# Optimization experiments

Measured on AMD Instinct MI355X. Metric: run time of the kernel, lower is better.

The kernel has to match this reference:

```python
import jax, jax.numpy as jnp
import numpy as np

NQ = 4          # n_qubits == hidden_dim (required for gate broadcasting)
D = 256         # embed_dim
H = 4           # num_heads
HD = D // H     # head_dim
V = 32000       # vocab
TAG = 64        # tagset_size
B, T = 16, 512


def _apply_rx(state, theta, wire):
    # state: (B, 2,2,2,2) complex64; theta: (B,) angles. RX = [[c,-is],[-is,c]], c=cos(t/2)
    half = theta * 0.5
    c = jnp.cos(half).reshape(-1, 1, 1, 1).astype(state.real.dtype)
    s = jnp.sin(half).reshape(-1, 1, 1, 1).astype(state.real.dtype)
    st = jnp.moveaxis(state, wire + 1, 1)
    a, b = st[:, 0], st[:, 1]
    st2 = jnp.stack([c * a - 1j * s * b, c * b - 1j * s * a], axis=1)
    return jnp.moveaxis(st2, 1, wire + 1)


def _apply_cnot(state, ctrl, tgt):
    st = jnp.moveaxis(state, (ctrl + 1, tgt + 1), (1, 2))
    st2 = jnp.stack([st[:, 0], st[:, 1, ::-1]], axis=1)  # flip target when ctrl=1
    return jnp.moveaxis(st2, (1, 2), (ctrl + 1, tgt + 1))


def _qlayer(angles, thetas):
    # angles: (B, NQ) data-encoding RX angles; thetas: (NQ,) trainable RX angles
    bsz = angles.shape[0]
    state = jnp.zeros((bsz,) + (2,) * NQ, jnp.complex64)
    state = state.at[(slice(None),) + (0,) * NQ].set(1.0)
    for w in range(NQ):
        state = _apply_rx(state, angles[:, w], w)
    for w in range(NQ):
        state = _apply_rx(state, jnp.broadcast_to(thetas[w], (bsz,)), w)
    for w in range(NQ - 1):
        state = _apply_cnot(state, w, w + 1)
    state = _apply_cnot(state, NQ - 1, 0)
    probs = state.real ** 2 + state.imag ** 2
    pm = jnp.array([1.0, -1.0], probs.dtype)
    outs = [
        jnp.sum(probs * pm.reshape((1,) + tuple(2 if i == w else 1 for i in range(NQ))),
                axis=tuple(range(1, NQ + 1)))
        for w in range(NQ)
    ]
    return jnp.stack(outs, axis=-1)  # (B, NQ) PauliZ expectations


def _forward(sentence, emb, Wq, bq, Wk, bk, Wv, bv, Wo, bo,
             Wf, bf, thf, Wi, bi, thi, Wg, bg, thg, Wo2, bo2, tho, Wt, bt):
    x = emb[sentence]  # (B, T, D)
    Bc, Tc, _ = x.shape
    # multi-head self-attention
    q = (x @ Wq.T + bq).reshape(Bc, Tc, H, HD).transpose(0, 2, 1, 3)
    k = (x @ Wk.T + bk).reshape(Bc, Tc, H, HD).transpose(0, 2, 1, 3)
    v = (x @ Wv.T + bv).reshape(Bc, Tc, H, HD).transpose(0, 2, 1, 3)
    scores = jnp.einsum('bhqd,bhkd->bhqk', q, k) / (HD ** 0.5)
    attn = jax.nn.softmax(scores, axis=-1)
    o = jnp.einsum('bhqk,bhkd->bhqd', attn, v).transpose(0, 2, 1, 3).reshape(Bc, Tc, D)
    attn_out = o @ Wo.T + bo  # (B, T, D)

    # quantum LSTM over time via scan
    def step(carry, x_t):
        hx, cx = carry  # (B, NQ) each
        comb = jnp.concatenate([x_t, hx], axis=-1)  # (B, D+NQ)
        f = jax.nn.sigmoid(_qlayer(comb @ Wf.T + bf, thf))
        i = jax.nn.sigmoid(_qlayer(comb @ Wi.T + bi, thi))
        g = jnp.tanh(_qlayer(comb @ Wg.T + bg, thg))
        oo = jax.nn.sigmoid(_qlayer(comb @ Wo2.T + bo2, tho))
        cx = f * cx + i * g
        hx = oo * jnp.tanh(cx)
        return (hx, cx), hx

    h0 = jnp.zeros((Bc, NQ), x.dtype)
    _, hs = jax.lax.scan(step, (h0, h0), attn_out.transpose(1, 0, 2))  # (T, B, NQ)
    lstm_out = hs.transpose(1, 0, 2)  # (B, T, NQ)
    logits = lstm_out @ Wt.T + bt
    return jax.nn.log_softmax(logits, axis=-1)


def setup_inputs() -> dict:
    key = jax.random.key(0)
    ks = jax.random.split(key, 24)
    n = lambda k, shp, sc=0.02: (jax.random.normal(k, shp, jnp.float32) * sc)
    DQ = D + NQ
    return {
        'sentence': jax.random.randint(ks[0], (B, T), 0, V),
        'emb': n(ks[1], (V, D), 1.0),
        'Wq': n(ks[2], (D, D)), 'bq': jnp.zeros((D,), jnp.float32),
        'Wk': n(ks[3], (D, D)), 'bk': jnp.zeros((D,), jnp.float32),
        'Wv': n(ks[4], (D, D)), 'bv': jnp.zeros((D,), jnp.float32),
        'Wo': n(ks[5], (D, D)), 'bo': jnp.zeros((D,), jnp.float32),
        'Wf': n(ks[6], (NQ, DQ), 0.05), 'bf': jnp.zeros((NQ,), jnp.float32),
        'thf': jax.random.uniform(ks[7], (NQ,), jnp.float32, 0.0, 2 * np.pi),
        'Wi': n(ks[8], (NQ, DQ), 0.05), 'bi': jnp.zeros((NQ,), jnp.float32),
        'thi': jax.random.uniform(ks[9], (NQ,), jnp.float32, 0.0, 2 * np.pi),
        'Wg': n(ks[10], (NQ, DQ), 0.05), 'bg': jnp.zeros((NQ,), jnp.float32),
        'thg': jax.random.uniform(ks[11], (NQ,), jnp.float32, 0.0, 2 * np.pi),
        'Wo2': n(ks[12], (NQ, DQ), 0.05), 'bo2': jnp.zeros((NQ,), jnp.float32),
        'tho': jax.random.uniform(ks[13], (NQ,), jnp.float32, 0.0, 2 * np.pi),
        'Wt': n(ks[14], (TAG, NQ), 0.1), 'bt': jnp.zeros((TAG,), jnp.float32),
    }


def reference(sentence, emb, Wq, bq, Wk, bk, Wv, bv, Wo, bo,
              Wf, bf, thf, Wi, bi, thi, Wg, bg, thg, Wo2, bo2, tho, Wt, bt):
    return _forward(sentence, emb, Wq, bq, Wk, bk, Wv, bv, Wo, bo,
                    Wf, bf, thf, Wi, bi, thi, Wg, bg, thg, Wo2, bo2, tho, Wt, bt)
```

## Files before the change

kernel.cpp:

```cpp
#include <hip/hip_runtime.h>
#include <hip/hip_bf16.h>

#define NB 16
#define NT 512
#define ND 256
#define NH 4
#define NHD 64
#define NTAG 64

typedef short bf16x8 __attribute__((ext_vector_type(8)));
typedef float f32x4 __attribute__((ext_vector_type(4)));
union LdsVec { uint4 u; bf16x8 v; };

#define INV2PI 0.15915494309189535f

__device__ __forceinline__ float ldf(const void* p, int isbf, long i) {
  return isbf ? __bfloat162float(((const __hip_bfloat16*)p)[i])
              : ((const float*)p)[i];
}
__device__ __forceinline__ unsigned short bfbits(float f) {
  __hip_bfloat16 h = __float2bfloat16(f);
  union { __hip_bfloat16 h; unsigned short s; } u{h};
  return u.s;
}
__device__ __forceinline__ unsigned int pack2(float a, float b) {
  return ((unsigned int)bfbits(b) << 16) | bfbits(a);
}

template <int CTRL>
__device__ __forceinline__ float dppf(float v) {
  return __int_as_float(
      __builtin_amdgcn_update_dpp(0, __float_as_int(v), CTRL, 0xF, 0xF, false));
}

__device__ __forceinline__ float frcp(float x) {
#if __has_builtin(__builtin_amdgcn_rcpf)
  return __builtin_amdgcn_rcpf(x);
#else
  float r; asm("v_rcp_f32 %0, %1" : "=v"(r) : "v"(x)); return r;
#endif
}
__device__ __forceinline__ float fexp2(float x) {
#if __has_builtin(__builtin_amdgcn_exp2f)
  return __builtin_amdgcn_exp2f(x);
#else
  float r; asm("v_exp_f32 %0, %1" : "=v"(r) : "v"(x)); return r;
#endif
}
__device__ __forceinline__ float fcosr(float x) {
#if __has_builtin(__builtin_amdgcn_cosf)
  return __builtin_amdgcn_cosf(x);
#else
  float r; asm("v_cos_f32 %0, %1" : "=v"(r) : "v"(x)); return r;
#endif
}

__device__ __forceinline__ int detect_isbf(const void* buf, int nview) {
  __shared__ int s_big;
  if (threadIdx.x == 0) s_big = 0;
  __syncthreads();
  const __hip_bfloat16* p = (const __hip_bfloat16*)buf;
  int big = 0;
  for (int i = threadIdx.x; i < nview; i += blockDim.x) {
    float v = __bfloat162float(p[i]);
    if (fabsf(v) > 1e4f) big = 1;
  }
  if (big) atomicOr(&s_big, 1);
  __syncthreads();
  return s_big ? 0 : 1;
}

#define AST 264
#define BST 40
__global__ __launch_bounds__(256) void k_qkvc(
    const int* __restrict__ sent, const void* emb,
    const void* Wq, const void* Wk, const void* Wv,
    const void* bq, const void* bk, const void* bv,
    const void* Wo, const void* bo,
    const void* Wf, const void* Wi, const void* Wg, const void* Wo2,
    const void* bF, const void* bI, const void* bG, const void* bO,
    const void* thF, const void* thI, const void* thG, const void* thO,
    __hip_bfloat16* Qbf, __hip_bfloat16* Kbf, __hip_bfloat16* Vtbf,
    __hip_bfloat16* __restrict__ Mbf, float* __restrict__ P) {
  __shared__ __align__(16) unsigned short SH[64 * AST + 4 * 64 * BST];
  unsigned short* AS = SH;
  unsigned short* BS = SH + 64 * AST;
  int z = blockIdx.z;
  int tid = threadIdx.x;

  if (z == 3) {
    if (blockIdx.x >= 4) return;
    float (*WGs)[256] = (float(*)[256])SH;
    float* cs = (float*)BS;
    int isbf = detect_isbf(Wo, 4096);
    for (int e = tid; e < 4096; e += 256) {
      int oi = e >> 8, j = e & 255;
      int gate = oi >> 2, w = oi & 3;
      const void* Ws = (gate == 0) ? Wf : (gate == 1) ? Wi : (gate == 2) ? Wg : Wo2;
      WGs[oi][j] = ldf(Ws, isbf, (long)w * 260 + j);
    }
    __syncthreads();
    if (tid < 64) {
      int d = blockIdx.x * 64 + tid;
      float m[16];
#pragma unroll
      for (int oi = 0; oi < 16; ++oi) m[oi] = 0.f;
#pragma unroll 4
      for (int j = 0; j < 256; ++j) {
        float wo = ldf(Wo, isbf, (long)j * 256 + d);
#pragma unroll
        for (int oi = 0; oi < 16; ++oi) m[oi] += WGs[oi][j] * wo;
      }
#pragma unroll
      for (int oi = 0; oi < 16; ++oi)
        Mbf[oi * 256 + d] = __float2bfloat16(m[oi]);
    }
    if (tid < 16) {
      int gate = tid >> 2, w = tid & 3;
      float cc = 0.f;
      for (int j = 0; j < 256; ++j) cc += WGs[tid][j] * ldf(bo, isbf, j);
      const void* bsel = (gate == 0) ? bF : (gate == 1) ? bI : (gate == 2) ? bG : bO;
      const void* tsel = (gate == 0) ? thF : (gate == 1) ? thI : (gate == 2) ? thG : thO;
      cs[tid] = (cc + ldf(bsel, isbf, w) + ldf(tsel, isbf, w)) * INV2PI;
    }
    __syncthreads();
    long pb = (long)blockIdx.x * 32768;
    for (int i = tid; i < 32768; i += 256) P[pb + i] = cs[i & 15];
    return;
  }

  const void* W = (z == 0) ? Wq : (z == 1) ? Wk : Wv;
  const void* Bb = (z == 0) ? bq : (z == 1) ? bk : bv;
  __hip_bfloat16* O = (z == 0) ? Qbf : (z == 1) ? Kbf : Vtbf;
  int isbf = detect_isbf(W, 1024);

  int rowbase = blockIdx.x * 64;
  int wave = tid >> 6, lane = tid & 63;
  int li = lane & 15, quad = lane >> 4;
  int colbase = wave * 64;
  unsigned short* Bw = &BS[wave * 64 * BST];

  const float* Wf32 = (const float*)W;
  const __hip_bfloat16* Wb16 = (const __hip_bfloat16*)W;
  long wrow = (long)(colbase + lane) * 256;

  float4 bf[8];
  uint4 bb4[4];
  if (isbf) {
#pragma unroll
    for (int j = 0; j < 4; ++j) bb4[j] = *(const uint4*)&Wb16[wrow + j * 8];
  } else {
#pragma unroll
    for (int j = 0; j < 8; ++j) bf[j] = *(const float4*)&Wf32[wrow + j * 4];
  }

  {
    int srow = tid >> 2;
    int sc = (tid & 3) * 64;
    long tok = (long)sent[rowbase + srow];
    if (isbf) {
      const __hip_bfloat16* eb = (const __hip_bfloat16*)emb + tok * 256 + sc;
#pragma unroll
      for (int j = 0; j < 8; ++j)
        *(uint4*)&AS[srow * AST + sc + j * 8] = *(const uint4*)&eb[j * 8];
    } else {
      const float* ef = (const float*)emb + tok * 256 + sc;
#pragma unroll
      for (int j = 0; j < 8; ++j) {
        float4 lo = *(const float4*)&ef[j * 8];
        float4 hi = *(const float4*)&ef[j * 8 + 4];
        uint4 pk;
        pk.x = pack2(lo.x, lo.y); pk.y = pack2(lo.z, lo.w);
        pk.z = pack2(hi.x, hi.y); pk.w = pack2(hi.z, hi.w);
        *(uint4*)&AS[srow * AST + sc + j * 8] = pk;
      }
    }
  }
  __syncthreads();

  f32x4 acc[4][4];
#pragma unroll
  for (int mt = 0; mt < 4; ++mt)
#pragma unroll
    for (int nt = 0; nt < 4; ++nt) acc[mt][nt] = (f32x4){0.f, 0.f, 0.f, 0.f};

#pragma unroll
  for (int k0 = 0; k0 < 256; k0 += 32) {
    if (isbf) {
#pragma unroll
      for (int j = 0; j < 4; ++j)
        *(uint4*)&Bw[lane * BST + j * 8] = bb4[j];
    } else {
#pragma unroll
      for (int j = 0; j < 4; ++j) {
        uint4 pk;
        pk.x = pack2(bf[2 * j].x, bf[2 * j].y);
        pk.y = pack2(bf[2 * j].z, bf[2 * j].w);
        pk.z = pack2(bf[2 * j + 1].x, bf[2 * j + 1].y);
        pk.w = pack2(bf[2 * j + 1].z, bf[2 * j + 1].w);
        *(uint4*)&Bw[lane * BST + j * 8] = pk;
      }
    }
    if (k0 < 224) {
      if (isbf) {
#pragma unroll
        for (int j = 0; j < 4; ++j)
          bb4[j] = *(const uint4*)&Wb16[wrow + k0 + 32 + j * 8];
      } else {
#pragma unroll
        for (int j = 0; j < 8; ++j)
          bf[j] = *(const float4*)&Wf32[wrow + k0 + 32 + j * 4];
      }
    }
    LdsVec a[4], b[4];
#pragma unroll
    for (int mt = 0; mt < 4; ++mt)
      a[mt].u = *(const uint4*)&AS[(mt * 16 + li) * AST + k0 + quad * 8];
#pragma unroll
    for (int nt = 0; nt < 4; ++nt)
      b[nt].u = *(const uint4*)&Bw[(nt * 16 + li) * BST + quad * 8];
#pragma unroll
    for (int mt = 0; mt < 4; ++mt)
#pragma unroll
      for (int nt = 0; nt < 4; ++nt)
        acc[mt][nt] = __builtin_amdgcn_mfma_f32_16x16x32_bf16(
            a[mt].v, b[nt].v, acc[mt][nt], 0, 0, 0);
  }

  __syncthreads();
  if (z == 2) {
#pragma unroll
    for (int nt = 0; nt < 4; ++nt) {
      int col = colbase + nt * 16 + li;
      float bias = ldf(Bb, isbf, col);
#pragma unroll
      for (int mt = 0; mt < 4; ++mt)
#pragma unroll
        for (int reg = 0; reg < 4; ++reg)
          SH[col * 72 + mt * 16 + quad * 4 + reg] =
              bfbits(acc[mt][nt][reg] + bias);
    }
  } else {
#pragma unroll
    for (int nt = 0; nt < 4; ++nt) {
      int col = colbase + nt * 16 + li;
      float bias = ldf(Bb, isbf, col);
#pragma unroll
      for (int mt = 0; mt < 4; ++mt)
#pragma unroll
        for (int reg = 0; reg < 4; ++reg)
          SH[(mt * 16 + quad * 4 + reg) * AST + col] =
              bfbits(acc[mt][nt][reg] + bias);
    }
  }
  __syncthreads();
  int bb2 = blockIdx.x >> 3, ttb = (blockIdx.x & 7) * 64;
  if (z == 2) {
#pragma unroll
    for (int j = 0; j < 8; ++j) {
      int e = tid + j * 256;
      int hdcol = e >> 3, c8 = (e & 7) * 8;
      uint4 v = *(const uint4*)&SH[hdcol * 72 + c8];
      *(uint4*)((__hip_bfloat16*)O +
                ((long)(bb2 * 4 + (hdcol >> 6)) * 64 + (hdcol & 63)) * 512 +
                ttb + c8) = v;
    }
  } else {
#pragma unroll
    for (int j = 0; j < 8; ++j) {
      int e = tid + j * 256;
      int row = e >> 5, c8e = (e & 31) * 8;
      int h = c8e >> 6, hd = c8e & 63;
      uint4 v = *(const uint4*)&SH[row * AST + c8e];
      *(uint4*)((__hip_bfloat16*)O +
                ((long)(bb2 * 4 + h) * 512 + ttb + row) * 64 + hd) = v;
    }
  }
}

#define LSTR 72
__global__ __launch_bounds__(256) void k_attn(const __hip_bfloat16* __restrict__ Qg,
                                              const __hip_bfloat16* __restrict__ Kg,
                                              const __hip_bfloat16* __restrict__ Vtg,
                                              const __hip_bfloat16* __restrict__ Mbf,
                                              float* __restrict__ P) {
  __shared__ __align__(16) unsigned short Qs[64 * LSTR];
  __shared__ __align__(16) unsigned short Ks[64 * LSTR];
  __shared__ __align__(16) unsigned short Vts[64 * LSTR];
  __shared__ __align__(16) unsigned short Ps[64 * LSTR];
  int tid = threadIdx.x;
  int bh = blockIdx.x, qt = blockIdx.y;
  int wave = tid >> 6, lane = tid & 63, li = lane & 15, quad = lane >> 4;

  const __hip_bfloat16* Qb = Qg + ((long)bh * 512 + qt * 64) * 64;
#pragma unroll
  for (int c = 0; c < 2; ++c) {
    int idx = tid + c * 256;
    int r = idx >> 3, c8 = (idx & 7) * 8;
    *(uint4*)&Qs[r * LSTR + c8] = *(const uint4*)&Qb[(long)r * 64 + c8];
  }

  f32x4 accO[4];
  float mrow[4], lrow[4];
#pragma unroll
  for (int i = 0; i < 4; ++i) {
    accO[i] = (f32x4){0.f, 0.f, 0.f, 0.f};
    mrow[i] = -1e30f; lrow[i] = 0.f;
  }

  for (int kt = 0; kt < 8; ++kt) {
    __syncthreads();
    const __hip_bfloat16* Kb = Kg + ((long)bh * 512 + kt * 64) * 64;
#pragma unroll
    for (int c = 0; c < 2; ++c) {
      int idx = tid + c * 256;
      int r = idx >> 3, c8 = (idx & 7) * 8;
      *(uint4*)&Ks[r * LSTR + c8] = *(const uint4*)&Kb[(long)r * 64 + c8];
      *(uint4*)&Vts[r * LSTR + c8] =
          *(const uint4*)&Vtg[((long)bh * 64 + r) * 512 + kt * 64 + c8];
    }
    __syncthreads();

    f32x4 s[4];
#pragma unroll
    for (int nb = 0; nb < 4; ++nb) s[nb] = (f32x4){0.f, 0.f, 0.f, 0.f};
#pragma unroll
    for (int nb = 0; nb < 4; ++nb)
#pragma unroll
      for (int kc = 0; kc < 2; ++kc) {
        LdsVec a, b;
        a.u = *(const uint4*)&Qs[(wave * 16 + li) * LSTR + kc * 32 + quad * 8];
        b.u = *(const uint4*)&Ks[(nb * 16 + li) * LSTR + kc * 32 + quad * 8];
        s[nb] = __builtin_amdgcn_mfma_f32_16x16x32_bf16(a.v, b.v, s[nb], 0, 0, 0);
      }
#pragma unroll
    for (int nb = 0; nb < 4; ++nb) s[nb] *= 0.125f;

#pragma unroll
    for (int reg = 0; reg < 4; ++reg) {
      float rm = fmaxf(fmaxf(s[0][reg], s[1][reg]), fmaxf(s[2][reg], s[3][reg]));
      rm = fmaxf(rm, __shfl_xor(rm, 1));
      rm = fmaxf(rm, __shfl_xor(rm, 2));
      rm = fmaxf(rm, __shfl_xor(rm, 4));
      rm = fmaxf(rm, __shfl_xor(rm, 8));
      float mnew = fmaxf(mrow[reg], rm);
      float alpha = __expf(mrow[reg] - mnew);
      mrow[reg] = mnew;
      float psum = 0.f;
#pragma unroll
      for (int nb = 0; nb < 4; ++nb) {
        float p = __expf(s[nb][reg] - mnew);
        psum += p;
        Ps[(wave * 16 + quad * 4 + reg) * LSTR + nb * 16 + li] = bfbits(p);
      }
      psum += __shfl_xor(psum, 1);
      psum += __shfl_xor(psum, 2);
      psum += __shfl_xor(psum, 4);
      psum += __shfl_xor(psum, 8);
      lrow[reg] = lrow[reg] * alpha + psum;
#pragma unroll
      for (int db = 0; db < 4; ++db) accO[db][reg] *= alpha;
    }
    __syncthreads();

#pragma unroll
    for (int db = 0; db < 4; ++db)
#pragma unroll
      for (int kc = 0; kc < 2; ++kc) {
        LdsVec a, b;
        a.u = *(const uint4*)&Ps[(wave * 16 + li) * LSTR + kc * 32 + quad * 8];
        b.u = *(const uint4*)&Vts[(db * 16 + li) * LSTR + kc * 32 + quad * 8];
        accO[db] = __builtin_amdgcn_mfma_f32_16x16x32_bf16(a.v, b.v, accO[db], 0, 0, 0);
      }
  }

  int batch = bh >> 2, head = bh & 3;
  __syncthreads();
  if (tid < 128) {
    int r = tid >> 3, c8 = (tid & 7) * 8;
    *(uint4*)&Qs[r * LSTR + c8] = *(const uint4*)&Mbf[r * 256 + head * 64 + c8];
  }
#pragma unroll
  for (int reg = 0; reg < 4; ++reg) {
    float inv = 1.f / lrow[reg];
#pragma unroll
    for (int db = 0; db < 4; ++db)
      Ps[(wave * 16 + quad * 4 + reg) * LSTR + db * 16 + li] =
          bfbits(accO[db][reg] * inv);
  }
  __syncthreads();
  f32x4 pacc = (f32x4){0.f, 0.f, 0.f, 0.f};
#pragma unroll
  for (int kc = 0; kc < 2; ++kc) {
    LdsVec a, b;
    a.u = *(const uint4*)&Ps[(wave * 16 + li) * LSTR + kc * 32 + quad * 8];
    b.u = *(const uint4*)&Qs[li * LSTR + kc * 32 + quad * 8];
    pacc = __builtin_amdgcn_mfma_f32_16x16x32_bf16(a.v, b.v, pacc, 0, 0, 0);
  }
  long pbase = (long)(batch >> 2) * 32768 + (batch & 3) * 16 + li;
#pragma unroll
  for (int reg = 0; reg < 4; ++reg) {
    int t = qt * 64 + wave * 16 + quad * 4 + reg;
    atomicAdd(&P[pbase + (long)t * 64], pacc[reg] * INV2PI);
  }
}

#define SWEEPS 4
#define CHUNK 16
#define NCH 32

template <bool DIRB>
__device__ __forceinline__ void scan_sweeps(
    const float* __restrict__ Pb,
    int c, int G, int w,
    float rr0, float rr1, float rr2, float rr3,
    float kk, float e1, float mkm1,
    int s0, int s1, int s2, int s3,
    float (*bH)[NCH + 1][4], float (*bC)[NCH + 1][4],
    float* __restrict__ hsb) {
  float pcv[CHUNK];
#pragma unroll
  for (int j = 0; j < CHUNK; ++j)
    pcv[j] = Pb[(long)(c * CHUNK + j) * 64];

#pragma unroll 1
  for (int s = 0; s < SWEEPS; ++s) {
    int rd = s & 1, wr = rd ^ 1;
    float h0 = bH[rd][c][0], h1 = bH[rd][c][1];
    float h2 = bH[rd][c][2], h3 = bH[rd][c][3];
    float cx = bC[rd][c][w];
    float hx = 0.f;
#pragma unroll
    for (int u = 0; u < CHUNK; ++u) {
      float pc = pcv[u];
      float d01 = __builtin_fmaf(rr1, h1, __builtin_fmaf(rr0, h0, pc));
      float d23 = __builtin_fmaf(rr3, h3, rr2 * h2);
      float a = d01 + d23;
      float cth = fcosr(a);
      float c0 = dppf<0x00>(cth), c1 = dppf<0x55>(cth);
      float c2 = dppf<0xAA>(cth), c3 = dppf<0xFF>(cth);
      float p01 = c0 * c1, z23 = c2 * c3;
      float v = (w == 0) ? c1 * z23 : (w == 1) ? p01
              : (w == 2) ? p01 * c2 : p01 * z23;
      float val = __builtin_fmaf(kk, frcp(1.f + fexp2(e1 * v)), mkm1);
      float ra = dppf<0x124>(val);
      float rb = dppf<0x128>(val);
      float rc = dppf<0x12C>(val);
      float rot1 = DIRB ? ra : rc;
      float rot3 = DIRB ? rc : ra;
      float f = (s0 == 0) ? val : (s0 == 1) ? rot1 : (s0 == 2) ? rb : rot3;
      float i = (s1 == 0) ? val : (s1 == 1) ? rot1 : (s1 == 2) ? rb : rot3;
      float g = (s2 == 0) ? val : (s2 == 1) ? rot1 : (s2 == 2) ? rb : rot3;
      float o = (s3 == 0) ? val : (s3 == 1) ? rot1 : (s3 == 2) ? rb : rot3;
      cx = __builtin_fmaf(f, cx, i * g);
      float rt = frcp(1.f + fexp2(-2.88539008f * cx));
      hx = __builtin_fmaf(o + o, rt, -o);
      h0 = dppf<0x00>(hx); h1 = dppf<0x55>(hx);
      h2 = dppf<0xAA>(hx); h3 = dppf<0xFF>(hx);
      if (G == 0) hsb[(c * CHUNK + u) * 4 + w] = hx;
    }
    if (G == 0) {
      bH[wr][c + 1][w] = hx;
      bC[wr][c + 1][w] = cx;
    }
    __syncthreads();
  }
}

__global__ __launch_bounds__(512) void k_scanf(const float* __restrict__ P,
                                               const void* Wf, const void* Wi,
                                               const void* Wg, const void* Wo2,
                                               const void* Wt, const void* Bt,
                                               void* outp) {
  __shared__ float bH[2][NCH + 1][4];
  __shared__ float bC[2][NCH + 1][4];
  __shared__ __align__(16) float hsb[512 * 4];
  __shared__ float sWt[256];
  __shared__ float sBt[64];
  int tid = threadIdx.x;
  int b = blockIdx.x;
  int c = tid >> 4;
  int l16 = tid & 15;
  int G = l16 >> 2, w = l16 & 3;
  int lane = tid & 63;

  if (tid < 2 * (NCH + 1) * 4) {
    ((float*)bH)[tid] = 0.f;
    ((float*)bC)[tid] = 0.f;
  }

  const __hip_bfloat16* pw = (const __hip_bfloat16*)Wf;
  int big = 0;
  for (int i = lane; i < 1040; i += 64) {
    float v = __bfloat162float(pw[i]);
    if (fabsf(v) > 1e4f) big = 1;
  }
  int isbf = (__ballot(big) == 0ULL) ? 1 : 0;

  if (tid < 256) sWt[tid] = ldf(Wt, isbf, tid);
  else if (tid < 320) sBt[tid - 256] = ldf(Bt, isbf, tid - 256);

  int got = __builtin_amdgcn_update_dpp(0, lane, 0x124, 0xF, 0xF, false);
  int dir = __shfl((got == 9) ? 1 : 0, 5);
  const void* Wsel = (G == 0) ? Wf : (G == 1) ? Wi : (G == 2) ? Wg : Wo2;
  float rr0 = ldf(Wsel, isbf, (long)w * 260 + 256 + 0) * INV2PI;
  float rr1 = ldf(Wsel, isbf, (long)w * 260 + 256 + 1) * INV2PI;
  float rr2 = ldf(Wsel, isbf, (long)w * 260 + 256 + 2) * INV2PI;
  float rr3 = ldf(Wsel, isbf, (long)w * 260 + 256 + 3) * INV2PI;
  float kk = (G == 2) ? 2.f : 1.f;
  float e1 = -kk * 1.44269504f;
  float mkm1 = 1.f - kk;
  int s0 = (0 - G) & 3, s1 = (1 - G) & 3, s2 = (2 - G) & 3, s3 = (3 - G) & 3;

  const float* Pb = P + (long)(b >> 2) * 32768 + (b & 3) * 16 + l16;
  __syncthreads();

  if (dir)
    scan_sweeps<true>(Pb, c, G, w, rr0, rr1, rr2, rr3,
                      kk, e1, mkm1, s0, s1, s2, s3, bH, bC, hsb);
  else
    scan_sweeps<false>(Pb, c, G, w, rr0, rr1, rr2, rr3,
                       kk, e1, mkm1, s0, s1, s2, s3, bH, bC, hsb);

  float h0 = hsb[tid * 4 + 0], h1 = hsb[tid * 4 + 1];
  float h2 = hsb[tid * 4 + 2], h3 = hsb[tid * 4 + 3];
  float lg[64];
  float mx = -1e30f;
#pragma unroll
  for (int j = 0; j < 64; ++j) {
    float v = sBt[j]
            + h0 * sWt[j * 4 + 0] + h1 * sWt[j * 4 + 1]
            + h2 * sWt[j * 4 + 2] + h3 * sWt[j * 4 + 3];
    lg[j] = v;
    mx = fmaxf(mx, v);
  }
  float ssum = 0.f;
#pragma unroll
  for (int j = 0; j < 64; ++j) ssum += __expf(lg[j] - mx);
  float sub = mx + __logf(ssum);
  long rbase = ((long)b * 512 + tid) * 64;
  if (isbf) {
    __hip_bfloat16* ob = (__hip_bfloat16*)outp;
#pragma unroll
    for (int j0 = 0; j0 < 8; ++j0) {
      uint4 pk;
      pk.x = pack2(lg[j0 * 8 + 0] - sub, lg[j0 * 8 + 1] - sub);
      pk.y = pack2(lg[j0 * 8 + 2] - sub, lg[j0 * 8 + 3] - sub);
      pk.z = pack2(lg[j0 * 8 + 4] - sub, lg[j0 * 8 + 5] - sub);
      pk.w = pack2(lg[j0 * 8 + 6] - sub, lg[j0 * 8 + 7] - sub);
      *(uint4*)(ob + rbase + j0 * 8) = pk;
    }
  } else {
    float* of = (float*)outp;
#pragma unroll
    for (int j0 = 0; j0 < 16; ++j0) {
      float4 v4;
      v4.x = lg[j0 * 4 + 0] - sub; v4.y = lg[j0 * 4 + 1] - sub;
      v4.z = lg[j0 * 4 + 2] - sub; v4.w = lg[j0 * 4 + 3] - sub;
      *(float4*)(of + rbase + j0 * 4) = v4;
    }
  }
}

extern "C" void kernel_launch(void* const* d_in, const int* in_sizes, int n_in,
                              void* d_out, int out_size, void* d_ws, size_t ws_size,
                              hipStream_t stream) {
  const int* sent = (const int*)d_in[0];
  const void* emb = d_in[1];
  const void* Wq = d_in[2];  const void* bq = d_in[3];
  const void* Wk = d_in[4];  const void* bk = d_in[5];
  const void* Wv = d_in[6];  const void* bv = d_in[7];
  const void* Wo = d_in[8];  const void* bo = d_in[9];
  const void* Wf = d_in[10]; const void* bF = d_in[11]; const void* thF = d_in[12];
  const void* Wi = d_in[13]; const void* bI = d_in[14]; const void* thI = d_in[15];
  const void* Wg = d_in[16]; const void* bG = d_in[17]; const void* thG = d_in[18];
  const void* Wo2 = d_in[19]; const void* bO = d_in[20]; const void* thO = d_in[21];
  const void* Wt = d_in[22]; const void* Bt = d_in[23];

  float* base = (float*)((char*)d_ws + 256);
  __hip_bfloat16* Mbf = (__hip_bfloat16*)base;
  __hip_bfloat16* Qbf  = (__hip_bfloat16*)(base + 4096);
  __hip_bfloat16* Kbf  = (__hip_bfloat16*)(base + 4096 + 1048576);
  __hip_bfloat16* Vtbf = (__hip_bfloat16*)(base + 4096 + 2097152);
  float* Pp = base + 4096 + 3145728;

  dim3 gq(128, 1, 4);
  k_qkvc<<<gq, 256, 0, stream>>>(sent, emb, Wq, Wk, Wv, bq, bk, bv, Wo, bo,
                                 Wf, Wi, Wg, Wo2, bF, bI, bG, bO,
                                 thF, thI, thG, thO, Qbf, Kbf, Vtbf, Mbf, Pp);
  dim3 ga(64, 8, 1);
  k_attn<<<ga, 256, 0, stream>>>(Qbf, Kbf, Vtbf, Mbf, Pp);
  k_scanf<<<16, 512, 0, stream>>>(Pp, Wf, Wi, Wg, Wo2, Wt, Bt, d_out);
}
```

Baseline: 231.9 us.

## Fuse K/V projection into attention kernel with per-head LDS-resident K and V

The K and V projections move out of the QKV kernel into a new attention kernel, with one 512-thread block per (batch, head). Each block computes the full K and transposed V for its head into XOR-swizzled LDS, then runs flash attention over all 512 queries from that resident K/V. This drops the global write and re-read of K and V and one launch's worth of work. The cost is only 64 blocks with about 144KB of LDS each, so GPU occupancy is much lower and the whole attention runs on a quarter of the CUs.

```diff
diff --git a/kernel.cpp b/kernel.cpp
--- a/kernel.cpp
+++ b/kernel.cpp
@@ -13,6 +13,7 @@
 union LdsVec { uint4 u; bf16x8 v; };
 
 #define INV2PI 0.15915494309189535f
+#define FSW(r, bc) ((bc) ^ (((r) & 7) << 4))
 
 __device__ __forceinline__ float ldf(const void* p, int isbf, long i) {
   return isbf ? __bfloat162float(((const __hip_bfloat16*)p)[i])
@@ -72,23 +73,21 @@
 
 #define AST 264
 #define BST 40
-__global__ __launch_bounds__(256) void k_qkvc(
+__global__ __launch_bounds__(256) void k_qc(
     const int* __restrict__ sent, const void* emb,
-    const void* Wq, const void* Wk, const void* Wv,
-    const void* bq, const void* bk, const void* bv,
+    const void* Wq, const void* bq,
     const void* Wo, const void* bo,
     const void* Wf, const void* Wi, const void* Wg, const void* Wo2,
     const void* bF, const void* bI, const void* bG, const void* bO,
     const void* thF, const void* thI, const void* thG, const void* thO,
-    __hip_bfloat16* Qbf, __hip_bfloat16* Kbf, __hip_bfloat16* Vtbf,
+    __hip_bfloat16* __restrict__ Qbf,
     __hip_bfloat16* __restrict__ Mbf, float* __restrict__ P) {
   __shared__ __align__(16) unsigned short SH[64 * AST + 4 * 64 * BST];
   unsigned short* AS = SH;
   unsigned short* BS = SH + 64 * AST;
-  int z = blockIdx.z;
   int tid = threadIdx.x;
 
-  if (z == 3) {
+  if (blockIdx.z == 1) {
     if (blockIdx.x >= 4) return;
     float (*WGs)[256] = (float(*)[256])SH;
     float* cs = (float*)BS;
@@ -129,19 +128,15 @@
     return;
   }
 
-  const void* W = (z == 0) ? Wq : (z == 1) ? Wk : Wv;
-  const void* Bb = (z == 0) ? bq : (z == 1) ? bk : bv;
-  __hip_bfloat16* O = (z == 0) ? Qbf : (z == 1) ? Kbf : Vtbf;
-  int isbf = detect_isbf(W, 1024);
-
+  int isbf = detect_isbf(Wq, 1024);
   int rowbase = blockIdx.x * 64;
   int wave = tid >> 6, lane = tid & 63;
   int li = lane & 15, quad = lane >> 4;
   int colbase = wave * 64;
   unsigned short* Bw = &BS[wave * 64 * BST];
 
-  const float* Wf32 = (const float*)W;
-  const __hip_bfloat16* Wb16 = (const __hip_bfloat16*)W;
+  const float* Wf32 = (const float*)Wq;
+  const __hip_bfloat16* Wb16 = (const __hip_bfloat16*)Wq;
   long wrow = (long)(colbase + lane) * 256;
 
   float4 bf[8];
@@ -228,180 +223,258 @@
   }
 
   __syncthreads();
-  if (z == 2) {
-#pragma unroll
-    for (int nt = 0; nt < 4; ++nt) {
-      int col = colbase + nt * 16 + li;
-      float bias = ldf(Bb, isbf, col);
-#pragma unroll
-      for (int mt = 0; mt < 4; ++mt)
-#pragma unroll
-        for (int reg = 0; reg < 4; ++reg)
-          SH[col * 72 + mt * 16 + quad * 4 + reg] =
-              bfbits(acc[mt][nt][reg] + bias);
-    }
-  } else {
-#pragma unroll
-    for (int nt = 0; nt < 4; ++nt) {
-      int col = colbase + nt * 16 + li;
-      float bias = ldf(Bb, isbf, col);
-#pragma unroll
-      for (int mt = 0; mt < 4; ++mt)
-#pragma unroll
-        for (int reg = 0; reg < 4; ++reg)
-          SH[(mt * 16 + quad * 4 + reg) * AST + col] =
-              bfbits(acc[mt][nt][reg] + bias);
-    }
+#pragma unroll
+  for (int nt = 0; nt < 4; ++nt) {
+    int col = colbase + nt * 16 + li;
+    float bias = ldf(bq, isbf, col);
+#pragma unroll
+    for (int mt = 0; mt < 4; ++mt)
+#pragma unroll
+      for (int reg = 0; reg < 4; ++reg)
+        SH[(mt * 16 + quad * 4 + reg) * AST + col] =
+            bfbits(acc[mt][nt][reg] + bias);
   }
   __syncthreads();
   int bb2 = blockIdx.x >> 3, ttb = (blockIdx.x & 7) * 64;
-  if (z == 2) {
-#pragma unroll
-    for (int j = 0; j < 8; ++j) {
-      int e = tid + j * 256;
-      int hdcol = e >> 3, c8 = (e & 7) * 8;
-      uint4 v = *(const uint4*)&SH[hdcol * 72 + c8];
-      *(uint4*)((__hip_bfloat16*)O +
-                ((long)(bb2 * 4 + (hdcol >> 6)) * 64 + (hdcol & 63)) * 512 +
-                ttb + c8) = v;
-    }
-  } else {
-#pragma unroll
-    for (int j = 0; j < 8; ++j) {
-      int e = tid + j * 256;
-      int row = e >> 5, c8e = (e & 31) * 8;
-      int h = c8e >> 6, hd = c8e & 63;
-      uint4 v = *(const uint4*)&SH[row * AST + c8e];
-      *(uint4*)((__hip_bfloat16*)O +
-                ((long)(bb2 * 4 + h) * 512 + ttb + row) * 64 + hd) = v;
-    }
-  }
-}
-
-#define LSTR 72
-__global__ __launch_bounds__(256) void k_attn(const __hip_bfloat16* __restrict__ Qg,
-                                              const __hip_bfloat16* __restrict__ Kg,
-                                              const __hip_bfloat16* __restrict__ Vtg,
-                                              const __hip_bfloat16* __restrict__ Mbf,
-                                              float* __restrict__ P) {
-  __shared__ __align__(16) unsigned short Qs[64 * LSTR];
-  __shared__ __align__(16) unsigned short Ks[64 * LSTR];
-  __shared__ __align__(16) unsigned short Vts[64 * LSTR];
-  __shared__ __align__(16) unsigned short Ps[64 * LSTR];
+#pragma unroll
+  for (int j = 0; j < 8; ++j) {
+    int e = tid + j * 256;
+    int row = e >> 5, c8e = (e & 31) * 8;
+    int h = c8e >> 6, hd = c8e & 63;
+    uint4 v = *(const uint4*)&SH[row * AST + c8e];
+    *(uint4*)(Qbf + ((long)(bb2 * 4 + h) * 512 + ttb + row) * 64 + hd) = v;
+  }
+}
+
+__global__ __launch_bounds__(512) void k_fat(
+    const int* __restrict__ sent, const void* emb,
+    const void* Wk, const void* Wv, const void* bk, const void* bv,
+    const __hip_bfloat16* __restrict__ Qg,
+    const __hip_bfloat16* __restrict__ Mbf, float* __restrict__ P) {
+  __shared__ __align__(16) unsigned char Ks[512 * 128];
+  __shared__ __align__(16) unsigned char Vts[64 * 1024];
+  __shared__ __align__(16) unsigned char AW[32 * 512];
   int tid = threadIdx.x;
-  int bh = blockIdx.x, qt = blockIdx.y;
   int wave = tid >> 6, lane = tid & 63, li = lane & 15, quad = lane >> 4;
-
-  const __hip_bfloat16* Qb = Qg + ((long)bh * 512 + qt * 64) * 64;
-#pragma unroll
-  for (int c = 0; c < 2; ++c) {
-    int idx = tid + c * 256;
-    int r = idx >> 3, c8 = (idx & 7) * 8;
-    *(uint4*)&Qs[r * LSTR + c8] = *(const uint4*)&Qb[(long)r * 64 + c8];
-  }
-
-  f32x4 accO[4];
-  float mrow[4], lrow[4];
-#pragma unroll
-  for (int i = 0; i < 4; ++i) {
-    accO[i] = (f32x4){0.f, 0.f, 0.f, 0.f};
-    mrow[i] = -1e30f; lrow[i] = 0.f;
-  }
-
-  for (int kt = 0; kt < 8; ++kt) {
+  int bh = blockIdx.x, batch = bh >> 2, head = bh & 3;
+  int isbf = detect_isbf(Wk, 1024);
+
+  int srow = tid >> 4, sseg = tid & 15;
+
+  int kvw = (wave < 4) ? wave : wave - 4;
+  int dloc = kvw * 16 + li;
+  int col = head * 64 + dloc;
+  const void* Wsel = (wave < 4) ? Wk : Wv;
+  float bias = ldf((wave < 4) ? bk : bv, isbf, col);
+  uint4 wf[8];
+  {
+    long wr = (long)col * 256;
+    if (isbf) {
+      const __hip_bfloat16* wp = (const __hip_bfloat16*)Wsel;
+#pragma unroll
+      for (int k0 = 0; k0 < 8; ++k0)
+        wf[k0] = *(const uint4*)&wp[wr + k0 * 32 + quad * 8];
+    } else {
+      const float* wp = (const float*)Wsel;
+#pragma unroll
+      for (int k0 = 0; k0 < 8; ++k0) {
+        const float* pp = wp + wr + k0 * 32 + quad * 8;
+        float4 lo = *(const float4*)pp, hi = *(const float4*)(pp + 4);
+        wf[k0].x = pack2(lo.x, lo.y); wf[k0].y = pack2(lo.z, lo.w);
+        wf[k0].z = pack2(hi.x, hi.y); wf[k0].w = pack2(hi.z, hi.w);
+      }
+    }
+  }
+
+  uint4 sa0, sa1;
+  {
+    long tok = (long)sent[batch * 512 + srow];
+    if (isbf) {
+      const __hip_bfloat16* ep = (const __hip_bfloat16*)emb + tok * 256;
+      sa0 = *(const uint4*)&ep[sseg * 8];
+      sa1 = *(const uint4*)&ep[(sseg + 16) * 8];
+    } else {
+      const float* ep = (const float*)emb + tok * 256;
+      const float* p0 = ep + sseg * 8;
+      float4 lo = *(const float4*)p0, hi = *(const float4*)(p0 + 4);
+      sa0.x = pack2(lo.x, lo.y); sa0.y = pack2(lo.z, lo.w);
+      sa0.z = pack2(hi.x, hi.y); sa0.w = pack2(hi.z, hi.w);
+      const float* p1 = ep + (sseg + 16) * 8;
+      lo = *(const float4*)p1; hi = *(const float4*)(p1 + 4);
+      sa1.x = pack2(lo.x, lo.y); sa1.y = pack2(lo.z, lo.w);
+      sa1.z = pack2(hi.x, hi.y); sa1.w = pack2(hi.z, hi.w);
+    }
+  }
+#pragma unroll 1
+  for (int hc = 0; hc < 16; ++hc) {
     __syncthreads();
-    const __hip_bfloat16* Kb = Kg + ((long)bh * 512 + kt * 64) * 64;
-#pragma unroll
-    for (int c = 0; c < 2; ++c) {
-      int idx = tid + c * 256;
-      int r = idx >> 3, c8 = (idx & 7) * 8;
-      *(uint4*)&Ks[r * LSTR + c8] = *(const uint4*)&Kb[(long)r * 64 + c8];
-      *(uint4*)&Vts[r * LSTR + c8] =
-          *(const uint4*)&Vtg[((long)bh * 64 + r) * 512 + kt * 64 + c8];
+    *(uint4*)(AW + srow * 512 + FSW(srow, sseg * 16)) = sa0;
+    *(uint4*)(AW + srow * 512 + FSW(srow, (sseg + 16) * 16)) = sa1;
+    if (hc < 15) {
+      long tok = (long)sent[batch * 512 + (hc + 1) * 32 + srow];
+      if (isbf) {
+        const __hip_bfloat16* ep = (const __hip_bfloat16*)emb + tok * 256;
+        sa0 = *(const uint4*)&ep[sseg * 8];
+        sa1 = *(const uint4*)&ep[(sseg + 16) * 8];
+      } else {
+        const float* ep = (const float*)emb + tok * 256;
+        const float* p0 = ep + sseg * 8;
+        float4 lo = *(const float4*)p0, hi = *(const float4*)(p0 + 4);
+        sa0.x = pack2(lo.x, lo.y); sa0.y = pack2(lo.z, lo.w);
+        sa0.z = pack2(hi.x, hi.y); sa0.w = pack2(hi.z, hi.w);
+        const float* p1 = ep + (sseg + 16) * 8;
+        lo = *(const float4*)p1; hi = *(const float4*)(p1 + 4);
+        sa1.x = pack2(lo.x, lo.y); sa1.y = pack2(lo.z, lo.w);
+        sa1.z = pack2(hi.x, hi.y); sa1.w = pack2(hi.z, hi.w);
+      }
     }
     __syncthreads();
-
-    f32x4 s[4];
-#pragma unroll
-    for (int nb = 0; nb < 4; ++nb) s[nb] = (f32x4){0.f, 0.f, 0.f, 0.f};
-#pragma unroll
-    for (int nb = 0; nb < 4; ++nb)
-#pragma unroll
-      for (int kc = 0; kc < 2; ++kc) {
-        LdsVec a, b;
-        a.u = *(const uint4*)&Qs[(wave * 16 + li) * LSTR + kc * 32 + quad * 8];
-        b.u = *(const uint4*)&Ks[(nb * 16 + li) * LSTR + kc * 32 + quad * 8];
-        s[nb] = __builtin_amdgcn_mfma_f32_16x16x32_bf16(a.v, b.v, s[nb], 0, 0, 0);
-      }
-#pragma unroll
-    for (int nb = 0; nb < 4; ++nb) s[nb] *= 0.125f;
-
-#pragma unroll
-    for (int reg = 0; reg < 4; ++reg) {
-      float rm = fmaxf(fmaxf(s[0][reg], s[1][reg]), fmaxf(s[2][reg], s[3][reg]));
-      rm = fmaxf(rm, __shfl_xor(rm, 1));
-      rm = fmaxf(rm, __shfl_xor(rm, 2));
-      rm = fmaxf(rm, __shfl_xor(rm, 4));
-      rm = fmaxf(rm, __shfl_xor(rm, 8));
-      float mnew = fmaxf(mrow[reg], rm);
-      float alpha = __expf(mrow[reg] - mnew);
-      mrow[reg] = mnew;
-      float psum = 0.f;
-#pragma unroll
-      for (int nb = 0; nb < 4; ++nb) {
-        float p = __expf(s[nb][reg] - mnew);
-        psum += p;
-        Ps[(wave * 16 + quad * 4 + reg) * LSTR + nb * 16 + li] = bfbits(p);
-      }
-      psum += __shfl_xor(psum, 1);
-      psum += __shfl_xor(psum, 2);
-      psum += __shfl_xor(psum, 4);
-      psum += __shfl_xor(psum, 8);
-      lrow[reg] = lrow[reg] * alpha + psum;
-#pragma unroll
-      for (int db = 0; db < 4; ++db) accO[db][reg] *= alpha;
-    }
-    __syncthreads();
-
-#pragma unroll
-    for (int db = 0; db < 4; ++db)
-#pragma unroll
-      for (int kc = 0; kc < 2; ++kc) {
-        LdsVec a, b;
-        a.u = *(const uint4*)&Ps[(wave * 16 + li) * LSTR + kc * 32 + quad * 8];
-        b.u = *(const uint4*)&Vts[(db * 16 + li) * LSTR + kc * 32 + quad * 8];
-        accO[db] = __builtin_amdgcn_mfma_f32_16x16x32_bf16(a.v, b.v, accO[db], 0, 0, 0);
-      }
-  }
-
-  int batch = bh >> 2, head = bh & 3;
+    int r0 = hc * 32;
+    f32x4 acc0 = (f32x4){0.f, 0.f, 0.f, 0.f};
+    f32x4 acc1 = (f32x4){0.f, 0.f, 0.f, 0.f};
+#pragma unroll
+    for (int k0 = 0; k0 < 8; ++k0) {
+      LdsVec a0, a1, b;
+      a0.u = *(const uint4*)(AW + li * 512 + FSW(li, k0 * 64 + quad * 16));
+      a1.u = *(const uint4*)(AW + (16 + li) * 512 + FSW(16 + li, k0 * 64 + quad * 16));
+      b.u = wf[k0];
+      acc0 = __builtin_amdgcn_mfma_f32_16x16x32_bf16(a0.v, b.v, acc0, 0, 0, 0);
+      acc1 = __builtin_amdgcn_mfma_f32_16x16x32_bf16(a1.v, b.v, acc1, 0, 0, 0);
+    }
+    if (wave < 4) {
+#pragma unroll
+      for (int reg = 0; reg < 4; ++reg) {
+        int t0 = r0 + quad * 4 + reg, t1 = t0 + 16;
+        *(unsigned short*)(Ks + t0 * 128 + FSW(t0, 2 * dloc)) =
+            bfbits(acc0[reg] + bias);
+        *(unsigned short*)(Ks + t1 * 128 + FSW(t1, 2 * dloc)) =
+            bfbits(acc1[reg] + bias);
+      }
+    } else {
+      uint2 p0, p1;
+      p0.x = pack2(acc0[0] + bias, acc0[1] + bias);
+      p0.y = pack2(acc0[2] + bias, acc0[3] + bias);
+      p1.x = pack2(acc1[0] + bias, acc1[1] + bias);
+      p1.y = pack2(acc1[2] + bias, acc1[3] + bias);
+      int t0 = r0 + quad * 4, t1 = t0 + 16;
+      *(uint2*)(Vts + dloc * 1024 + FSW(dloc, 2 * t0)) = p0;
+      *(uint2*)(Vts + dloc * 1024 + FSW(dloc, 2 * t1)) = p1;
+    }
+  }
   __syncthreads();
-  if (tid < 128) {
-    int r = tid >> 3, c8 = (tid & 7) * 8;
-    *(uint4*)&Qs[r * LSTR + c8] = *(const uint4*)&Mbf[r * 256 + head * 64 + c8];
-  }
-#pragma unroll
-  for (int reg = 0; reg < 4; ++reg) {
-    float inv = 1.f / lrow[reg];
-#pragma unroll
-    for (int db = 0; db < 4; ++db)
-      Ps[(wave * 16 + quad * 4 + reg) * LSTR + db * 16 + li] =
-          bfbits(accO[db][reg] * inv);
-  }
-  __syncthreads();
-  f32x4 pacc = (f32x4){0.f, 0.f, 0.f, 0.f};
-#pragma unroll
-  for (int kc = 0; kc < 2; ++kc) {
-    LdsVec a, b;
-    a.u = *(const uint4*)&Ps[(wave * 16 + li) * LSTR + kc * 32 + quad * 8];
-    b.u = *(const uint4*)&Qs[li * LSTR + kc * 32 + quad * 8];
-    pacc = __builtin_amdgcn_mfma_f32_16x16x32_bf16(a.v, b.v, pacc, 0, 0, 0);
-  }
+
+  unsigned char* rg = AW + wave * 2048;
+  uint4 mf0 = *(const uint4*)&Mbf[li * 256 + head * 64 + 0 * 32 + quad * 8];
+  uint4 mf1 = *(const uint4*)&Mbf[li * 256 + head * 64 + 1 * 32 + quad * 8];
   long pbase = (long)(batch >> 2) * 32768 + (batch & 3) * 16 + li;
-#pragma unroll
-  for (int reg = 0; reg < 4; ++reg) {
-    int t = qt * 64 + wave * 16 + quad * 4 + reg;
-    atomicAdd(&P[pbase + (long)t * 64], pacc[reg] * INV2PI);
+
+#pragma unroll 1
+  for (int qh = 0; qh < 2; ++qh) {
+    uint4 qf[2][2];
+#pragma unroll
+    for (int mt = 0; mt < 2; ++mt)
+#pragma unroll
+      for (int kc = 0; kc < 2; ++kc)
+        qf[mt][kc] = *(const uint4*)&Qg[((long)bh * 512 + wave * 64 + qh * 32 +
+                                         mt * 16 + li) * 64 + kc * 32 + quad * 8];
+    f32x4 accO[2][4];
+    float mrow[2][4], lrow[2][4];
+#pragma unroll
+    for (int mt = 0; mt < 2; ++mt)
+#pragma unroll
+      for (int db = 0; db < 4; ++db) {
+        accO[mt][db] = (f32x4){0.f, 0.f, 0.f, 0.f};
+        mrow[mt][db] = -1e30f; lrow[mt][db] = 0.f;
+      }
+
+#pragma unroll 1
+    for (int kt = 0; kt < 8; ++kt) {
+      f32x4 s[2][4];
+#pragma unroll
+      for (int mt = 0; mt < 2; ++mt)
+#pragma unroll
+        for (int nb = 0; nb < 4; ++nb) s[mt][nb] = (f32x4){0.f, 0.f, 0.f, 0.f};
+#pragma unroll
+      for (int nb = 0; nb < 4; ++nb)
+#pragma unroll
+        for (int kc = 0; kc < 2; ++kc) {
+          int tr = kt * 64 + nb * 16 + li;
+          LdsVec b, a0, a1;
+          b.u = *(const uint4*)(Ks + tr * 128 + FSW(tr, kc * 64 + quad * 16));
+          a0.u = qf[0][kc]; a1.u = qf[1][kc];
+          s[0][nb] = __builtin_amdgcn_mfma_f32_16x16x32_bf16(a0.v, b.v, s[0][nb], 0, 0, 0);
+          s[1][nb] = __builtin_amdgcn_mfma_f32_16x16x32_bf16(a1.v, b.v, s[1][nb], 0, 0, 0);
+        }
+#pragma unroll
+      for (int mt = 0; mt < 2; ++mt) {
+#pragma unroll
+        for (int nb = 0; nb < 4; ++nb) s[mt][nb] *= 0.125f;
+#pragma unroll
+        for (int reg = 0; reg < 4; ++reg) {
+          float rm = fmaxf(fmaxf(s[mt][0][reg], s[mt][1][reg]),
+                           fmaxf(s[mt][2][reg], s[mt][3][reg]));
+          rm = fmaxf(rm, __shfl_xor(rm, 1));
+          rm = fmaxf(rm, __shfl_xor(rm, 2));
+          rm = fmaxf(rm, __shfl_xor(rm, 4));
+          rm = fmaxf(rm, __shfl_xor(rm, 8));
+          float mnew = fmaxf(mrow[mt][reg], rm);
+          float alpha = __expf(mrow[mt][reg] - mnew);
+          mrow[mt][reg] = mnew;
+          float psum = 0.f;
+#pragma unroll
+          for (int nb = 0; nb < 4; ++nb) {
+            float p = __expf(s[mt][nb][reg] - mnew);
+            psum += p;
+            *(unsigned short*)(rg + (quad * 4 + reg) * 128 +
+                               FSW(quad * 4 + reg, 2 * (nb * 16 + li))) = bfbits(p);
+          }
+          psum += __shfl_xor(psum, 1);
+          psum += __shfl_xor(psum, 2);
+          psum += __shfl_xor(psum, 4);
+          psum += __shfl_xor(psum, 8);
+          lrow[mt][reg] = lrow[mt][reg] * alpha + psum;
+#pragma unroll
+          for (int db = 0; db < 4; ++db) accO[mt][db][reg] *= alpha;
+        }
+        LdsVec pa0, pa1;
+        pa0.u = *(const uint4*)(rg + li * 128 + FSW(li, quad * 16));
+        pa1.u = *(const uint4*)(rg + li * 128 + FSW(li, 64 + quad * 16));
+#pragma unroll
+        for (int db = 0; db < 4; ++db) {
+          int vd = db * 16 + li;
+          LdsVec b0, b1;
+          b0.u = *(const uint4*)(Vts + vd * 1024 + FSW(vd, kt * 128 + quad * 16));
+          b1.u = *(const uint4*)(Vts + vd * 1024 + FSW(vd, kt * 128 + 64 + quad * 16));
+          accO[mt][db] = __builtin_amdgcn_mfma_f32_16x16x32_bf16(pa0.v, b0.v, accO[mt][db], 0, 0, 0);
+          accO[mt][db] = __builtin_amdgcn_mfma_f32_16x16x32_bf16(pa1.v, b1.v, accO[mt][db], 0, 0, 0);
+        }
+      }
+    }
+
+#pragma unroll
+    for (int mt = 0; mt < 2; ++mt) {
+#pragma unroll
+      for (int reg = 0; reg < 4; ++reg) {
+        float inv = frcp(lrow[mt][reg]);
+#pragma unroll
+        for (int db = 0; db < 4; ++db)
+          *(unsigned short*)(rg + (quad * 4 + reg) * 128 +
+                             FSW(quad * 4 + reg, 2 * (db * 16 + li))) =
+              bfbits(accO[mt][db][reg] * inv);
+      }
+      LdsVec a0, a1, m0, m1;
+      a0.u = *(const uint4*)(rg + li * 128 + FSW(li, quad * 16));
+      a1.u = *(const uint4*)(rg + li * 128 + FSW(li, 64 + quad * 16));
+      m0.u = mf0; m1.u = mf1;
+      f32x4 pacc = (f32x4){0.f, 0.f, 0.f, 0.f};
+      pacc = __builtin_amdgcn_mfma_f32_16x16x32_bf16(a0.v, m0.v, pacc, 0, 0, 0);
+      pacc = __builtin_amdgcn_mfma_f32_16x16x32_bf16(a1.v, m1.v, pacc, 0, 0, 0);
+#pragma unroll
+      for (int reg = 0; reg < 4; ++reg) {
+        int t = wave * 64 + qh * 32 + mt * 16 + quad * 4 + reg;
+        atomicAdd(&P[pbase + (long)t * 64], pacc[reg] * INV2PI);
+      }
+    }
   }
 }
 
@@ -579,16 +652,13 @@
 
   float* base = (float*)((char*)d_ws + 256);
   __hip_bfloat16* Mbf = (__hip_bfloat16*)base;
-  __hip_bfloat16* Qbf  = (__hip_bfloat16*)(base + 4096);
-  __hip_bfloat16* Kbf  = (__hip_bfloat16*)(base + 4096 + 1048576);
-  __hip_bfloat16* Vtbf = (__hip_bfloat16*)(base + 4096 + 2097152);
-  float* Pp = base + 4096 + 3145728;
-
-  dim3 gq(128, 1, 4);
-  k_qkvc<<<gq, 256, 0, stream>>>(sent, emb, Wq, Wk, Wv, bq, bk, bv, Wo, bo,
-                                 Wf, Wi, Wg, Wo2, bF, bI, bG, bO,
-                                 thF, thI, thG, thO, Qbf, Kbf, Vtbf, Mbf, Pp);
-  dim3 ga(64, 8, 1);
-  k_attn<<<ga, 256, 0, stream>>>(Qbf, Kbf, Vtbf, Mbf, Pp);
+  __hip_bfloat16* Qbf = (__hip_bfloat16*)(base + 4096);
+  float* Pp = base + 4096 + 1048576;
+
+  dim3 gq(128, 1, 2);
+  k_qc<<<gq, 256, 0, stream>>>(sent, emb, Wq, bq, Wo, bo,
+                               Wf, Wi, Wg, Wo2, bF, bI, bG, bO,
+                               thF, thI, thG, thO, Qbf, Mbf, Pp);
+  k_fat<<<64, 512, 0, stream>>>(sent, emb, Wk, Wv, bk, bv, Qbf, Mbf, Pp);
   k_scanf<<<16, 512, 0, stream>>>(Pp, Wf, Wi, Wg, Wo2, Wt, Bt, d_out);
 }
```

New measurement: 279.1 us. 20.4% more time.

## Replace per-head atomic accumulation with per-head partial buffers summed in scan

Applied to the files above, without the earlier changes.

The attention kernel used to atomically add each head's gate pre-activation contribution into a shared P buffer that the setup kernel had first filled with constants. It now writes each head's partial as a plain float4 store into its own slice of a time-contiguous layout. The scan kernel sums the four head slices with vector loads and adds a per-gate constant read from a small buffer. This removes the atomics and the 128K-float prefill, at the cost of four times more partial-buffer reads in the serial scan kernel.

```diff
diff --git a/kernel.cpp b/kernel.cpp
--- a/kernel.cpp
+++ b/kernel.cpp
@@ -81,7 +81,7 @@
     const void* bF, const void* bI, const void* bG, const void* bO,
     const void* thF, const void* thI, const void* thG, const void* thO,
     __hip_bfloat16* Qbf, __hip_bfloat16* Kbf, __hip_bfloat16* Vtbf,
-    __hip_bfloat16* __restrict__ Mbf, float* __restrict__ P) {
+    __hip_bfloat16* __restrict__ Mbf, float* __restrict__ cvb) {
   __shared__ __align__(16) unsigned short SH[64 * AST + 4 * 64 * BST];
   unsigned short* AS = SH;
   unsigned short* BS = SH + 64 * AST;
@@ -91,7 +91,6 @@
   if (z == 3) {
     if (blockIdx.x >= 4) return;
     float (*WGs)[256] = (float(*)[256])SH;
-    float* cs = (float*)BS;
     int isbf = detect_isbf(Wo, 4096);
     for (int e = tid; e < 4096; e += 256) {
       int oi = e >> 8, j = e & 255;
@@ -115,17 +114,14 @@
       for (int oi = 0; oi < 16; ++oi)
         Mbf[oi * 256 + d] = __float2bfloat16(m[oi]);
     }
-    if (tid < 16) {
+    if (blockIdx.x == 0 && tid < 16) {
       int gate = tid >> 2, w = tid & 3;
       float cc = 0.f;
       for (int j = 0; j < 256; ++j) cc += WGs[tid][j] * ldf(bo, isbf, j);
       const void* bsel = (gate == 0) ? bF : (gate == 1) ? bI : (gate == 2) ? bG : bO;
       const void* tsel = (gate == 0) ? thF : (gate == 1) ? thI : (gate == 2) ? thG : thO;
-      cs[tid] = (cc + ldf(bsel, isbf, w) + ldf(tsel, isbf, w)) * INV2PI;
-    }
-    __syncthreads();
-    long pb = (long)blockIdx.x * 32768;
-    for (int i = tid; i < 32768; i += 256) P[pb + i] = cs[i & 15];
+      cvb[tid] = (cc + ldf(bsel, isbf, w) + ldf(tsel, isbf, w)) * INV2PI;
+    }
     return;
   }
 
@@ -397,12 +393,13 @@
     b.u = *(const uint4*)&Qs[li * LSTR + kc * 32 + quad * 8];
     pacc = __builtin_amdgcn_mfma_f32_16x16x32_bf16(a.v, b.v, pacc, 0, 0, 0);
   }
-  long pbase = (long)(batch >> 2) * 32768 + (batch & 3) * 16 + li;
-#pragma unroll
-  for (int reg = 0; reg < 4; ++reg) {
-    int t = qt * 64 + wave * 16 + quad * 4 + reg;
-    atomicAdd(&P[pbase + (long)t * 64], pacc[reg] * INV2PI);
-  }
+  int pblk = batch >> 2, brow = (batch & 3) * 16 + li;
+  long off = ((long)((head * 4 + pblk) * 64 + brow)) * 512 +
+             qt * 64 + wave * 16 + quad * 4;
+  float4 st;
+  st.x = pacc[0] * INV2PI; st.y = pacc[1] * INV2PI;
+  st.z = pacc[2] * INV2PI; st.w = pacc[3] * INV2PI;
+  *(float4*)&P[off] = st;
 }
 
 #define SWEEPS 4
@@ -411,7 +408,7 @@
 
 template <bool DIRB>
 __device__ __forceinline__ void scan_sweeps(
-    const float* __restrict__ Pb,
+    const float* __restrict__ Pb, float cvv,
     int c, int G, int w,
     float rr0, float rr1, float rr2, float rr3,
     float kk, float e1, float mkm1,
@@ -420,8 +417,16 @@
     float* __restrict__ hsb) {
   float pcv[CHUNK];
 #pragma unroll
-  for (int j = 0; j < CHUNK; ++j)
-    pcv[j] = Pb[(long)(c * CHUNK + j) * 64];
+  for (int j4 = 0; j4 < CHUNK / 4; ++j4) {
+    float4 a = *(const float4*)&Pb[0 * 131072 + c * 16 + j4 * 4];
+    float4 b = *(const float4*)&Pb[1 * 131072 + c * 16 + j4 * 4];
+    float4 d = *(const float4*)&Pb[2 * 131072 + c * 16 + j4 * 4];
+    float4 e = *(const float4*)&Pb[3 * 131072 + c * 16 + j4 * 4];
+    pcv[j4 * 4 + 0] = cvv + a.x + b.x + d.x + e.x;
+    pcv[j4 * 4 + 1] = cvv + a.y + b.y + d.y + e.y;
+    pcv[j4 * 4 + 2] = cvv + a.z + b.z + d.z + e.z;
+    pcv[j4 * 4 + 3] = cvv + a.w + b.w + d.w + e.w;
+  }
 
 #pragma unroll 1
   for (int s = 0; s < SWEEPS; ++s) {
@@ -468,6 +473,7 @@
 }
 
 __global__ __launch_bounds__(512) void k_scanf(const float* __restrict__ P,
+                                               const float* __restrict__ cvb,
                                                const void* Wf, const void* Wi,
                                                const void* Wg, const void* Wo2,
                                                const void* Wt, const void* Bt,
@@ -512,14 +518,15 @@
   float mkm1 = 1.f - kk;
   int s0 = (0 - G) & 3, s1 = (1 - G) & 3, s2 = (2 - G) & 3, s3 = (3 - G) & 3;
 
-  const float* Pb = P + (long)(b >> 2) * 32768 + (b & 3) * 16 + l16;
+  const float* Pb = P + ((long)(b >> 2) * 64 + (b & 3) * 16 + l16) * 512;
+  float cvv = cvb[l16];
   __syncthreads();
 
   if (dir)
-    scan_sweeps<true>(Pb, c, G, w, rr0, rr1, rr2, rr3,
+    scan_sweeps<true>(Pb, cvv, c, G, w, rr0, rr1, rr2, rr3,
                       kk, e1, mkm1, s0, s1, s2, s3, bH, bC, hsb);
   else
-    scan_sweeps<false>(Pb, c, G, w, rr0, rr1, rr2, rr3,
+    scan_sweeps<false>(Pb, cvv, c, G, w, rr0, rr1, rr2, rr3,
                        kk, e1, mkm1, s0, s1, s2, s3, bH, bC, hsb);
 
   float h0 = hsb[tid * 4 + 0], h1 = hsb[tid * 4 + 1];
@@ -579,6 +586,7 @@
 
   float* base = (float*)((char*)d_ws + 256);
   __hip_bfloat16* Mbf = (__hip_bfloat16*)base;
+  float* cvb = base + 2048;
   __hip_bfloat16* Qbf  = (__hip_bfloat16*)(base + 4096);
   __hip_bfloat16* Kbf  = (__hip_bfloat16*)(base + 4096 + 1048576);
   __hip_bfloat16* Vtbf = (__hip_bfloat16*)(base + 4096 + 2097152);
@@ -587,8 +595,8 @@
   dim3 gq(128, 1, 4);
   k_qkvc<<<gq, 256, 0, stream>>>(sent, emb, Wq, Wk, Wv, bq, bk, bv, Wo, bo,
                                  Wf, Wi, Wg, Wo2, bF, bI, bG, bO,
-                                 thF, thI, thG, thO, Qbf, Kbf, Vtbf, Mbf, Pp);
+                                 thF, thI, thG, thO, Qbf, Kbf, Vtbf, Mbf, cvb);
   dim3 ga(64, 8, 1);
   k_attn<<<ga, 256, 0, stream>>>(Qbf, Kbf, Vtbf, Mbf, Pp);
-  k_scanf<<<16, 512, 0, stream>>>(Pp, Wf, Wi, Wg, Wo2, Wt, Bt, d_out);
-}
+  k_scanf<<<16, 512, 0, stream>>>(Pp, cvb, Wf, Wi, Wg, Wo2, Wt, Bt, d_out);
+}
```

Result: no change. 230.7 us (-0.5%).
